# Kernel optimization log

Measured on AMD Instinct MI355X. Metric: run time of the kernel, lower is better.

## Reference

```python
import jax, jax.numpy as jnp
import numpy as np

B, S, D = 16, 2048, 768  # batch, padded subword length, roberta hidden dim


def setup_inputs() -> dict:
    key = jax.random.key(0)
    k1, k2 = jax.random.split(key)
    robert_embed = jax.random.normal(k1, (B, S, D), dtype=jnp.float32)
    # Non-decreasing per-row segment ids: contiguous runs of equal ids are the
    # subword spans that merge_list would average; singleton runs pass through.
    seg_ids = jnp.sort(jax.random.randint(k2, (B, S), 0, S, dtype=jnp.int32), axis=-1)
    return {"robert_embed": robert_embed, "seg_ids": seg_ids}


def reference(robert_embed, seg_ids):
    # Segment-mean gather/scatter: out[b, w] = mean_{p: seg_ids[b,p]==w} x[b, p]
    b, s, d = robert_embed.shape
    w = s  # output word slots (<= s); empty slots yield zeros
    flat_seg = (seg_ids + (w * jnp.arange(b, dtype=seg_ids.dtype))[:, None]).reshape(-1)
    x_flat = robert_embed.reshape(-1, d)
    sums = jax.ops.segment_sum(x_flat, flat_seg, num_segments=b * w)  # [b*w, d]
    counts = jax.ops.segment_sum(
        jnp.ones((b * s,), dtype=robert_embed.dtype), flat_seg, num_segments=b * w
    )
    out = sums / jnp.maximum(counts, 1)[:, None]
    return out.reshape(b, w, d)
```

## Files before the change

kernel.cpp:

```cpp
#include <hip/hip_runtime.h>

#define BB 16
#define SS 2048
#define DD 768
#define D4 (DD / 4)

__global__ __launch_bounds__(256) void seg_mean_fused(
    const float* __restrict__ x,
    const int*   __restrict__ seg,
    float*       __restrict__ out) {
    int lane = threadIdx.x & 63;
    int wave = threadIdx.x >> 6;
    int bw   = (blockIdx.x << 2) + wave;
    int b    = bw >> 11;
    int w    = bw & (SS - 1);
    const int* srow = seg + (b << 11);

    int lo = 0, n = SS;
    while (n > 0) {
        int half = n >> 1;
        int mid  = lo + half;
        if (srow[mid] < w) { lo = mid + 1; n -= half + 1; }
        else               { n = half; }
    }

    int c = 0;
    int p = lo;
    for (;;) {
        int idx = p + lane;
        int v   = (idx < SS) ? srow[idx] : -1;
        unsigned long long m = __ballot(v == w);
        unsigned long long nm = ~m;
        if (nm) { c += (int)__builtin_ctzll(nm); break; }
        c += 64; p += 64;
    }

    float4* outp = (float4*)(out + (size_t)bw * DD);
    if (c == 0) {
        float4 z = make_float4(0.f, 0.f, 0.f, 0.f);
        outp[lane]       = z;
        outp[lane + 64]  = z;
        outp[lane + 128] = z;
        return;
    }

    const float4* xp = (const float4*)(x + ((size_t)b * SS + (size_t)lo) * DD);
    float4 a0 = xp[lane];
    float4 a1 = xp[lane + 64];
    float4 a2 = xp[lane + 128];
    for (int j = 1; j < c; ++j) {
        const float4* xr = xp + (size_t)j * D4;
        float4 r0 = xr[lane], r1 = xr[lane + 64], r2 = xr[lane + 128];
        a0.x += r0.x; a0.y += r0.y; a0.z += r0.z; a0.w += r0.w;
        a1.x += r1.x; a1.y += r1.y; a1.z += r1.z; a1.w += r1.w;
        a2.x += r2.x; a2.y += r2.y; a2.z += r2.z; a2.w += r2.w;
    }
    float inv = 1.0f / (float)c;
    a0.x *= inv; a0.y *= inv; a0.z *= inv; a0.w *= inv;
    a1.x *= inv; a1.y *= inv; a1.z *= inv; a1.w *= inv;
    a2.x *= inv; a2.y *= inv; a2.z *= inv; a2.w *= inv;
    outp[lane]       = a0;
    outp[lane + 64]  = a1;
    outp[lane + 128] = a2;
}

extern "C" void kernel_launch(void* const* d_in, const int* in_sizes, int n_in,
                              void* d_out, int out_size, void* d_ws, size_t ws_size,
                              hipStream_t stream) {
    const float* x   = (const float*)d_in[0];
    const int*   seg = (const int*)d_in[1];
    float* out = (float*)d_out;

    int nBlocks = (BB * SS) / 4;
    seg_mean_fused<<<nBlocks, 256, 0, stream>>>(x, seg, out);
}
```

Measured before the change: 180.6 us.

## Share lower-bound searches per block and compute counts from adjacent bounds

Each block now handles 16 consecutive word slots. It runs 17 binary searches in parallel and keeps the bounds in shared memory, so each count is the difference of adjacent lower bounds. This replaces the per-wave binary search plus the ballot scan of segment ids. Each wave then processes four slots one after another, and outputs are written with nontemporal stores. The costs are fewer, larger blocks (2048 instead of 8192), serial per-wave work over four slots, and a __syncthreads.

```diff
diff --git a/kernel.cpp b/kernel.cpp
--- a/kernel.cpp
+++ b/kernel.cpp
@@ -4,64 +4,69 @@
 #define SS 2048
 #define DD 768
 #define D4 (DD / 4)
+#define SPB 16
+#define BLOCKS_PER_ROW (SS / SPB)
 
-__global__ __launch_bounds__(256) void seg_mean_fused(
+typedef float vfloat4 __attribute__((ext_vector_type(4)));
+
+__global__ __launch_bounds__(256) void seg_mean_v3(
     const float* __restrict__ x,
     const int*   __restrict__ seg,
     float*       __restrict__ out) {
+    __shared__ int sLb[SPB + 1];
+
+    int b  = blockIdx.x >> 7;
+    int w0 = (blockIdx.x & (BLOCKS_PER_ROW - 1)) << 4;
+    const int* srow = seg + (b << 11);
+
+    if (threadIdx.x <= SPB) {
+        int w  = w0 + threadIdx.x;
+        int lo = 0, n = SS;
+        while (n > 0) {
+            int half = n >> 1;
+            int mid  = lo + half;
+            if (srow[mid] < w) { lo = mid + 1; n -= half + 1; }
+            else               { n = half; }
+        }
+        sLb[threadIdx.x] = lo;
+    }
+    __syncthreads();
+
     int lane = threadIdx.x & 63;
     int wave = threadIdx.x >> 6;
-    int bw   = (blockIdx.x << 2) + wave;
-    int b    = bw >> 11;
-    int w    = bw & (SS - 1);
-    const int* srow = seg + (b << 11);
+    size_t rowBase = (size_t)(b << 11);
 
-    int lo = 0, n = SS;
-    while (n > 0) {
-        int half = n >> 1;
-        int mid  = lo + half;
-        if (srow[mid] < w) { lo = mid + 1; n -= half + 1; }
-        else               { n = half; }
+    for (int si = (wave << 2); si < (wave << 2) + 4; ++si) {
+        int st = sLb[si];
+        int c  = sLb[si + 1] - st;
+        vfloat4* outp = (vfloat4*)(out + (rowBase + (size_t)(w0 + si)) * DD);
+
+        if (c == 0) {
+            vfloat4 z = (vfloat4){0.f, 0.f, 0.f, 0.f};
+            __builtin_nontemporal_store(z, &outp[lane]);
+            __builtin_nontemporal_store(z, &outp[lane + 64]);
+            __builtin_nontemporal_store(z, &outp[lane + 128]);
+            continue;
+        }
+
+        const vfloat4* xp = (const vfloat4*)(x + (rowBase + (size_t)st) * DD);
+        vfloat4 a0 = xp[lane];
+        vfloat4 a1 = xp[lane + 64];
+        vfloat4 a2 = xp[lane + 128];
+        for (int j = 1; j < c; ++j) {
+            const vfloat4* xr = xp + (size_t)j * D4;
+            a0 += xr[lane];
+            a1 += xr[lane + 64];
+            a2 += xr[lane + 128];
+        }
+        float inv = 1.0f / (float)c;
+        a0 *= inv;
+        a1 *= inv;
+        a2 *= inv;
+        __builtin_nontemporal_store(a0, &outp[lane]);
+        __builtin_nontemporal_store(a1, &outp[lane + 64]);
+        __builtin_nontemporal_store(a2, &outp[lane + 128]);
     }
-
-    int c = 0;
-    int p = lo;
-    for (;;) {
-        int idx = p + lane;
-        int v   = (idx < SS) ? srow[idx] : -1;
-        unsigned long long m = __ballot(v == w);
-        unsigned long long nm = ~m;
-        if (nm) { c += (int)__builtin_ctzll(nm); break; }
-        c += 64; p += 64;
-    }
-
-    float4* outp = (float4*)(out + (size_t)bw * DD);
-    if (c == 0) {
-        float4 z = make_float4(0.f, 0.f, 0.f, 0.f);
-        outp[lane]       = z;
-        outp[lane + 64]  = z;
-        outp[lane + 128] = z;
-        return;
-    }
-
-    const float4* xp = (const float4*)(x + ((size_t)b * SS + (size_t)lo) * DD);
-    float4 a0 = xp[lane];
-    float4 a1 = xp[lane + 64];
-    float4 a2 = xp[lane + 128];
-    for (int j = 1; j < c; ++j) {
-        const float4* xr = xp + (size_t)j * D4;
-        float4 r0 = xr[lane], r1 = xr[lane + 64], r2 = xr[lane + 128];
-        a0.x += r0.x; a0.y += r0.y; a0.z += r0.z; a0.w += r0.w;
-        a1.x += r1.x; a1.y += r1.y; a1.z += r1.z; a1.w += r1.w;
-        a2.x += r2.x; a2.y += r2.y; a2.z += r2.z; a2.w += r2.w;
-    }
-    float inv = 1.0f / (float)c;
-    a0.x *= inv; a0.y *= inv; a0.z *= inv; a0.w *= inv;
-    a1.x *= inv; a1.y *= inv; a1.z *= inv; a1.w *= inv;
-    a2.x *= inv; a2.y *= inv; a2.z *= inv; a2.w *= inv;
-    outp[lane]       = a0;
-    outp[lane + 64]  = a1;
-    outp[lane + 128] = a2;
 }
 
 extern "C" void kernel_launch(void* const* d_in, const int* in_sizes, int n_in,
@@ -71,6 +76,6 @@
     const int*   seg = (const int*)d_in[1];
     float* out = (float*)d_out;
 
-    int nBlocks = (BB * SS) / 4;
-    seg_mean_fused<<<nBlocks, 256, 0, stream>>>(x, seg, out);
+    int nBlocks = BB * BLOCKS_PER_ROW;
+    seg_mean_v3<<<nBlocks, 256, 0, stream>>>(x, seg, out);
 }
```

Measured after the change: 185.3 us. 2.6% more time.
